# Optimization experiments

Measured on AMD Instinct MI355X. Metric: run time of the kernel, lower is better.

## Reference

```python
import jax, jax.numpy as jnp
import numpy as np

BS, NQ, NK = 2, 2048, 2048
D_OUT, H, D_K, D_V = 1024, 16, 64, 64


def _xavier(key, shape):
    fan_in, fan_out = shape[1], shape[0]
    lim = float(np.sqrt(6.0 / (fan_in + fan_out)))
    return jax.random.uniform(key, shape, jnp.float32, -lim, lim)


def setup_inputs() -> dict:
    key = jax.random.key(0)
    ks = jax.random.split(key, 9)
    return {
        "queries": jax.random.normal(ks[0], (BS, NQ, D_OUT), jnp.float32),
        "keys": jax.random.normal(ks[1], (BS, NK, D_OUT), jnp.float32),
        "values": jax.random.normal(ks[2], (BS, NK, D_OUT), jnp.float32),
        "mask": jax.random.randint(ks[3], (BS, H, NQ, NK), 0, 2).astype(bool),
        "weights": jax.random.uniform(ks[4], (BS, H, NQ, NK), jnp.float32),
        "Wq": _xavier(ks[5], (H * D_K, D_OUT)),
        "bq": jnp.zeros((H * D_K,), jnp.float32),
        "Wk": _xavier(ks[6], (H * D_K, D_OUT)),
        "bk": jnp.zeros((H * D_K,), jnp.float32),
        "Wv": _xavier(ks[7], (H * D_V, D_OUT)),
        "bv": jnp.zeros((H * D_V,), jnp.float32),
        "Wo": _xavier(ks[8], (D_OUT, H * D_V)),
        "bo": jnp.zeros((D_OUT,), jnp.float32),
    }


def reference(queries, keys, values, mask, weights, Wq, bq, Wk, bk, Wv, bv, Wo, bo):
    bs, nq, _ = queries.shape
    nk = keys.shape[1]
    # projections: (bs, n, h*d) -> (bs, h, n, d)
    q = (queries @ Wq.T + bq).reshape(bs, nq, H, D_K).transpose(0, 2, 1, 3)
    k = (keys @ Wk.T + bk).reshape(bs, nk, H, D_K).transpose(0, 2, 1, 3)
    v = (values @ Wv.T + bv).reshape(bs, nk, H, D_V).transpose(0, 2, 1, 3)
    # scaled dot-product scores: (bs, h, nq, nk)
    att = jnp.einsum("bhqd,bhkd->bhqk", q, k) / jnp.sqrt(jnp.float32(D_K))
    att = att * weights                      # elementwise weight bias
    att = jnp.where(mask, -jnp.inf, att)     # masked_fill(mask, -inf)
    att = jax.nn.softmax(att, axis=-1)
    # dropout is identity at p=0 / eval
    out = jnp.einsum("bhqk,bhkd->bhqd", att, v)  # (bs, h, nq, d_v)
    out = out.transpose(0, 2, 1, 3).reshape(bs, nq, H * D_V)
    return out @ Wo.T + bo
```

## Files before the change

### kernel.cpp

```cpp
#include <hip/hip_runtime.h>
#include <stdint.h>

#define DEV __device__ __forceinline__

typedef __attribute__((__ext_vector_type__(8))) short short8;
typedef __attribute__((__ext_vector_type__(4))) float f32x4;
typedef __attribute__((__ext_vector_type__(16))) float f32x16;
typedef __attribute__((__ext_vector_type__(4))) unsigned short ushort4_t;
typedef __attribute__((__ext_vector_type__(4))) _Float16 half4;
typedef __attribute__((__ext_vector_type__(8))) _Float16 half8;

DEV unsigned short f2bf(float f) {
  union { float f; unsigned u; } x; x.f = f;
  unsigned u = x.u;
  unsigned r = (u + 0x7FFFu + ((u >> 16) & 1u)) >> 16;
  return (unsigned short)r;
}

DEV unsigned short f2h(float f) {
  _Float16 h = (_Float16)f;
  unsigned short u;
  __builtin_memcpy(&u, &h, 2);
  return u;
}

DEV void gload_lds16(const void* g, void* l) {
  __builtin_amdgcn_global_load_lds(
      (const __attribute__((address_space(1))) unsigned int*)g,
      (__attribute__((address_space(3))) unsigned int*)l,
      16, 0, 0);
}

DEV short8 ld_g8(const unsigned short* p) { return *(const short8*)p; }
DEV short8 ld_s8(const unsigned short* p) { return *(const short8*)p; }
DEV half4 ld_h4(const unsigned short* p) {
  half4 r; __builtin_memcpy(&r, p, 8); return r;
}

__global__ void detect_mask_fmt(const unsigned int* __restrict__ mask, int* __restrict__ flag) {
  if (threadIdx.x == 0 && blockIdx.x == 0) {
    int fmt = 1;
    for (int i = 0; i < 256; ++i) {
      unsigned u = mask[i];
      if (u == 0x3F800000u) { fmt = 2; break; }
      if ((u & 0xFFFFFF00u) != 0u) { fmt = 0; break; }
    }
    *flag = fmt;
  }
}

__global__ void pack_mask(const unsigned char* __restrict__ m8,
                          const unsigned int* __restrict__ m32,
                          const int* __restrict__ mfmt,
                          unsigned int* __restrict__ pm) {
  __shared__ unsigned int tile[32 * 65];
  const int bh = blockIdx.x >> 6;
  const int q0 = (blockIdx.x & 63) * 32;
  const int fmt = *mfmt;
  const int tid = threadIdx.x;
#pragma unroll
  for (int rnd = 0; rnd < 8; ++rnd) {
    int w = tid + rnd * 256;
    int q = w >> 6, t = w & 63;
    size_t sb = ((size_t)(bh * 2048 + q0 + q)) * 2048 + t * 32;
    unsigned bits = 0;
    if (fmt == 0) {
      uint4 a = *(const uint4*)(m8 + sb);
      uint4 bq = *(const uint4*)(m8 + sb + 16);
      unsigned wa0 = a.x, wa1 = a.y, wa2 = a.z, wa3 = a.w;
      unsigned wb0 = bq.x, wb1 = bq.y, wb2 = bq.z, wb3 = bq.w;
#pragma unroll
      for (int e = 0; e < 4; ++e) {
        bits |= (((wa0 >> (8 * e)) & 0xFFu) ? 1u : 0u) << (0 + e);
        bits |= (((wa1 >> (8 * e)) & 0xFFu) ? 1u : 0u) << (4 + e);
        bits |= (((wa2 >> (8 * e)) & 0xFFu) ? 1u : 0u) << (8 + e);
        bits |= (((wa3 >> (8 * e)) & 0xFFu) ? 1u : 0u) << (12 + e);
        bits |= (((wb0 >> (8 * e)) & 0xFFu) ? 1u : 0u) << (16 + e);
        bits |= (((wb1 >> (8 * e)) & 0xFFu) ? 1u : 0u) << (20 + e);
        bits |= (((wb2 >> (8 * e)) & 0xFFu) ? 1u : 0u) << (24 + e);
        bits |= (((wb3 >> (8 * e)) & 0xFFu) ? 1u : 0u) << (28 + e);
      }
    } else {
#pragma unroll
      for (int c = 0; c < 8; ++c) {
        uint4 v = *(const uint4*)(m32 + sb + c * 4);
        bits |= (v.x ? 1u : 0u) << (c * 4);
        bits |= (v.y ? 1u : 0u) << (c * 4 + 1);
        bits |= (v.z ? 1u : 0u) << (c * 4 + 2);
        bits |= (v.w ? 1u : 0u) << (c * 4 + 3);
      }
    }
    tile[q * 65 + t] = bits;
  }
  __syncthreads();
#pragma unroll
  for (int rnd = 0; rnd < 8; ++rnd) {
    int w = tid + rnd * 256;
    int t = w >> 5, q = w & 31;
    pm[((size_t)bh * 64 + t) * 2048 + q0 + q] = tile[q * 65 + t];
  }
}

__global__ void cvt_all(const float* __restrict__ q, const float* __restrict__ k,
                        const float* __restrict__ v,
                        const float* __restrict__ wq, const float* __restrict__ wk,
                        const float* __restrict__ wv, const float* __restrict__ wo,
                        unsigned short* __restrict__ Xq, unsigned short* __restrict__ Xk,
                        unsigned short* __restrict__ Xv, unsigned short* __restrict__ Wqb,
                        unsigned short* __restrict__ Wkb, unsigned short* __restrict__ Wvb,
                        unsigned short* __restrict__ Wob) {
  int i = blockIdx.x * 256 + threadIdx.x;
  const float* src; unsigned short* dst; int off;
  if (i < 1048576)      { src = q;  dst = Xq;  off = i; }
  else if (i < 2097152) { src = k;  dst = Xk;  off = i - 1048576; }
  else if (i < 3145728) { src = v;  dst = Xv;  off = i - 2097152; }
  else if (i < 3407872) { src = wq; dst = Wqb; off = i - 3145728; }
  else if (i < 3670016) { src = wk; dst = Wkb; off = i - 3407872; }
  else if (i < 3932160) { src = wv; dst = Wvb; off = i - 3670016; }
  else                  { src = wo; dst = Wob; off = i - 3932160; }
  float4 vv = ((const float4*)src)[off];
  ushort4_t r;
  r.x = f2bf(vv.x); r.y = f2bf(vv.y); r.z = f2bf(vv.z); r.w = f2bf(vv.w);
  ((ushort4_t*)dst)[off] = r;
}

__global__ __launch_bounds__(256, 2) void proj_gemm(
    const unsigned short* __restrict__ Xq, const unsigned short* __restrict__ Xk,
    const unsigned short* __restrict__ Xv,
    const unsigned short* __restrict__ Wqb, const unsigned short* __restrict__ Wkb,
    const unsigned short* __restrict__ Wvb,
    const float* __restrict__ bq, const float* __restrict__ bk, const float* __restrict__ bv,
    unsigned short* __restrict__ QP, unsigned short* __restrict__ KP,
    unsigned short* __restrict__ VT) {
  const int tid = threadIdx.x;
// ... 30 lines not shown
    __syncthreads();

    short8 af[4], bfr[4];
#pragma unroll
    for (int i = 0; i < 4; ++i)
      af[i] = ld_s8(&stage[aoff + (wm + i * 16 + l16) * 32 + hi * 8]);
#pragma unroll
    for (int j = 0; j < 4; ++j)
      bfr[j] = ld_s8(&stage[boff + (wn + j * 16 + l16) * 32 + hi * 8]);
#pragma unroll
    for (int i = 0; i < 4; ++i)
#pragma unroll
      for (int j = 0; j < 4; ++j)
        acc[i][j] = __builtin_amdgcn_mfma_f32_16x16x32_bf16(af[i], bfr[j], acc[i][j], 0, 0, 0);
    __syncthreads();
  }

  if (sel != 2) {
#pragma unroll
    for (int j = 0; j < 4; ++j) {
      int feat = n0 + wn + j * 16 + l16;
      float bi = bias[feat];
      int h = feat >> 6, d = feat & 63;
#pragma unroll
      for (int i = 0; i < 4; ++i) {
#pragma unroll
        for (int r = 0; r < 4; ++r) {
          int m = m0 + wm + i * 16 + hi * 4 + r;
          int b = m >> 11, n = m & 2047;
          float v = acc[i][j][r] + bi;
          out[(((size_t)(b * 16 + h)) * 2048 + n) * 64 + d] = f2bf(v);
        }
      }
    }
  } else {
#pragma unroll
    for (int j = 0; j < 4; ++j) {
      int tc0 = m0 + wn + j * 16;
      int b = tc0 >> 11, n = tc0 & 2047;
#pragma unroll
      for (int i = 0; i < 4; ++i) {
#pragma unroll
        for (int r = 0; r < 4; ++r) {
          int feat = n0 + wm + i * 16 + hi * 4 + r;
          int h = feat >> 6, d = feat & 63;
          float v = acc[i][j][r] + bias[feat];
          out[((size_t)(b * 16 + h) * 64 + d) * 2048 + n + l16] = f2h(v);
        }
      }
    }
  }
}

__global__ __launch_bounds__(256, 2) void attn_kernel(
    const unsigned short* __restrict__ Q, const unsigned short* __restrict__ K,
    const unsigned short* __restrict__ VT,
    const float* __restrict__ weights,
    const unsigned int* __restrict__ pm,
    unsigned short* __restrict__ O) {
  const int bid = blockIdx.x;
  const int qt = bid >> 5, bh = bid & 31;
  const int b = bh >> 4, h = bh & 15;
  const int tid = threadIdx.x, wid = tid >> 6, lane = tid & 63;
  const int l31 = lane & 31, hh = lane >> 5;
  const size_t bh_nd = (size_t)bh * 2048 * 64;
  const int q0 = qt * 128;
  const int qg = q0 + wid * 32 + l31;

  short8 qf0 = ld_g8(Q + bh_nd + (size_t)qg * 64 + 0  + hh * 8);
  short8 qf1 = ld_g8(Q + bh_nd + (size_t)qg * 64 + 16 + hh * 8);
  short8 qf2 = ld_g8(Q + bh_nd + (size_t)qg * 64 + 32 + hh * 8);
  short8 qf3 = ld_g8(Q + bh_nd + (size_t)qg * 64 + 48 + hh * 8);

  __shared__ float wlds[2][128 * 32];
  __shared__ unsigned short vlds[2][64 * 32];

  const float* wsrc = weights + (size_t)bh * 2048 * 2048;
  const unsigned short* vsrc = VT + bh_nd;
  const int wswz = 4 * ((lane & 7) ^ (lane >> 3));
  const int vswz = 8 * ((lane & 3) ^ ((lane >> 3) & 3));
  const int wrow_s = q0 + wid * 32 + (lane >> 3);
  const int vrow_s = wid * 16 + (lane >> 2);

#define STAGE(NXT, KT)                                                        \
  {                                                                           \
    _Pragma("unroll")                                                         \
    for (int i = 0; i < 4; ++i)                                               \
      gload_lds16(wsrc + (size_t)(wrow_s + i * 8) * 2048 + (KT) + wswz,       \
                  &wlds[NXT][(wid * 4 + i) * 256]);                           \
    gload_lds16(vsrc + (size_t)vrow_s * 2048 + (KT) + vswz,                   \
                &vlds[NXT][wid * 512]);                                       \
  }

  f32x16 o0 = {}, o1 = {};
  float mrow = -1e30f, lrow = 0.f;

  STAGE(0, 0)
  __syncthreads();

  for (int t = 0; t < 64; ++t) {
    const int cur = t & 1;
    const int kt0 = t * 32;

    short8 kf0 = ld_g8(K + bh_nd + (size_t)(kt0 + l31) * 64 + 0  + hh * 8);
    short8 kf1 = ld_g8(K + bh_nd + (size_t)(kt0 + l31) * 64 + 16 + hh * 8);
    short8 kf2 = ld_g8(K + bh_nd + (size_t)(kt0 + l31) * 64 + 32 + hh * 8);
    short8 kf3 = ld_g8(K + bh_nd + (size_t)(kt0 + l31) * 64 + 48 + hh * 8);
    unsigned mw = pm[((size_t)bh * 64 + t) * 2048 + qg];

    if (t < 63) STAGE(cur ^ 1, kt0 + 32)

    f32x16 s = {};
    s = __builtin_amdgcn_mfma_f32_32x32x16_bf16(kf0, qf0, s, 0, 0, 0);
    s = __builtin_amdgcn_mfma_f32_32x32x16_bf16(kf1, qf1, s, 0, 0, 0);
    s = __builtin_amdgcn_mfma_f32_32x32x16_bf16(kf2, qf2, s, 0, 0, 0);
    s = __builtin_amdgcn_mfma_f32_32x32x16_bf16(kf3, qf3, s, 0, 0, 0);

    const float* wrow = &wlds[cur][(wid * 32 + l31) * 32];
    f32x4 wv[4];
    wv[0] = *(const f32x4*)&wrow[4 * ((hh + 0) ^ (l31 & 7))];
    wv[1] = *(const f32x4*)&wrow[4 * ((hh + 2) ^ (l31 & 7))];
    wv[2] = *(const f32x4*)&wrow[4 * ((hh + 4) ^ (l31 & 7))];
    wv[3] = *(const f32x4*)&wrow[4 * ((hh + 6) ^ (l31 & 7))];

    unsigned mb = mw >> (4 * hh);
#pragma unroll
    for (int r = 0; r < 16; ++r) {
      bool mk = (mb >> ((r & 3) + 8 * (r >> 2))) & 1;
      s[r] = mk ? -INFINITY : s[r] * 0.125f * wv[r >> 2][r & 3];
    }

    float tm = s[0];
#pragma unroll
    for (int r = 1; r < 16; ++r) tm = fmaxf(tm, s[r]);
    float tm2 = fmaxf(tm, __shfl_xor(tm, 32));
    if (__any(tm2 > mrow)) {
      float mnew = fmaxf(mrow, tm2);
      float sc = __expf(mrow - mnew);
      lrow *= sc;
      o0 *= sc;
      o1 *= sc;
      mrow = mnew;
    }
    float ps = 0.f;
#pragma unroll
    for (int r = 0; r < 16; ++r) {
      s[r] = __expf(s[r] - mrow);
      ps += s[r];
    }
    lrow += ps;

    half8 pa0, pa1;
#pragma unroll
    for (int r = 0; r < 8; ++r) {
      pa0[r] = (_Float16)s[r];
      pa1[r] = (_Float16)s[8 + r];
    }

    {
      const unsigned short* vr = &vlds[cur][l31 * 32];
      half4 a0 = ld_h4(&vr[4 * ((hh + 0) ^ (l31 & 6))]);
      half4 a1 = ld_h4(&vr[4 * ((hh + 2) ^ (l31 & 6))]);
      half8 vf;
#pragma unroll
      for (int e = 0; e < 4; ++e) { vf[e] = a0[e]; vf[4 + e] = a1[e]; }
      o0 = __builtin_amdgcn_mfma_f32_32x32x16_f16(vf, pa0, o0, 0, 0, 0);
      half4 b0 = ld_h4(&vr[4 * ((hh + 4) ^ (l31 & 6))]);
      half4 b1 = ld_h4(&vr[4 * ((hh + 6) ^ (l31 & 6))]);
#pragma unroll
      for (int e = 0; e < 4; ++e) { vf[e] = b0[e]; vf[4 + e] = b1[e]; }
      o0 = __builtin_amdgcn_mfma_f32_32x32x16_f16(vf, pa1, o0, 0, 0, 0);
    }
    {
      const unsigned short* vr = &vlds[cur][(32 + l31) * 32];
      half4 a0 = ld_h4(&vr[4 * ((hh + 0) ^ (l31 & 6))]);
      half4 a1 = ld_h4(&vr[4 * ((hh + 2) ^ (l31 & 6))]);
      half8 vf;
#pragma unroll
      for (int e = 0; e < 4; ++e) { vf[e] = a0[e]; vf[4 + e] = a1[e]; }
      o1 = __builtin_amdgcn_mfma_f32_32x32x16_f16(vf, pa0, o1, 0, 0, 0);
      half4 b0 = ld_h4(&vr[4 * ((hh + 4) ^ (l31 & 6))]);
      half4 b1 = ld_h4(&vr[4 * ((hh + 6) ^ (l31 & 6))]);
#pragma unroll
      for (int e = 0; e < 4; ++e) { vf[e] = b0[e]; vf[4 + e] = b1[e]; }
      o1 = __builtin_amdgcn_mfma_f32_32x32x16_f16(vf, pa1, o1, 0, 0, 0);
    }

    __syncthreads();
  }

  lrow += __shfl_xor(lrow, 32);
  float inv = 1.0f / lrow;
  const size_t ob = (size_t)(b * 2048 + qg) * 1024 + h * 64;
#pragma unroll
  for (int j = 0; j < 4; ++j) {
    ushort4_t pk;
    pk.x = f2bf(o0[4 * j + 0] * inv); pk.y = f2bf(o0[4 * j + 1] * inv);
    pk.z = f2bf(o0[4 * j + 2] * inv); pk.w = f2bf(o0[4 * j + 3] * inv);
    *(ushort4_t*)&O[ob + 8 * j + 4 * hh] = pk;
    ushort4_t pk1;
    pk1.x = f2bf(o1[4 * j + 0] * inv); pk1.y = f2bf(o1[4 * j + 1] * inv);
    pk1.z = f2bf(o1[4 * j + 2] * inv); pk1.w = f2bf(o1[4 * j + 3] * inv);
    *(ushort4_t*)&O[ob + 32 + 8 * j + 4 * hh] = pk1;
  }
#undef STAGE
}

__global__ __launch_bounds__(256, 2) void out_gemm(
    const unsigned short* __restrict__ A, const unsigned short* __restrict__ W,
    const float* __restrict__ bias, float* __restrict__ Cout) {
  const int tid = threadIdx.x;
  const int wid = tid >> 6, lane = tid & 63;
  const int l16 = lane & 15, hi = lane >> 4;
  const int m0 = blockIdx.x * 128;
  const int n0 = blockIdx.y * 128;

  __shared__ unsigned short stage[2 * 128 * 32];
  f32x4 acc[4][4] = {};
  const int wm = (wid >> 1) * 64, wn = (wid & 1) * 64;

  for (int kt = 0; kt < 1024; kt += 32) {
#pragma unroll
    for (int t = 0; t < 4; ++t) {
      int g = wid * 4 + t;
      int c = g & 7;
      int row = c * 16 + (lane >> 2);
      int ko = (lane & 3) * 8;
      const unsigned short* src = (g < 8)
          ? (A + (size_t)(m0 + row) * 1024 + kt + ko)
          : (W + (size_t)(n0 + row) * 1024 + kt + ko);
      gload_lds16(src, (unsigned short*)((char*)stage + g * 1024));
    }
    __syncthreads();

    short8 af[4], bfr[4];
#pragma unroll
    for (int i = 0; i < 4; ++i)
      af[i] = ld_s8(&stage[(wm + i * 16 + l16) * 32 + hi * 8]);
#pragma unroll
    for (int j = 0; j < 4; ++j)
      bfr[j] = ld_s8(&stage[4096 + (wn + j * 16 + l16) * 32 + hi * 8]);
#pragma unroll
    for (int i = 0; i < 4; ++i)
#pragma unroll
      for (int j = 0; j < 4; ++j)
        acc[i][j] = __builtin_amdgcn_mfma_f32_16x16x32_bf16(af[i], bfr[j], acc[i][j], 0, 0, 0);
    __syncthreads();
  }

#pragma unroll
  for (int j = 0; j < 4; ++j) {
    int feat = n0 + wn + j * 16 + l16;
    float bi = bias[feat];
#pragma unroll
    for (int i = 0; i < 4; ++i) {
#pragma unroll
      for (int r = 0; r < 4; ++r) {
        int m = m0 + wm + i * 16 + hi * 4 + r;
        Cout[(size_t)m * 1024 + feat] = acc[i][j][r] + bi;
      }
    }
  }
}

extern "C" void kernel_launch(void* const* d_in, const int* in_sizes, int n_in,
                              void* d_out, int out_size, void* d_ws, size_t ws_size,
                              hipStream_t stream) {
  const float* queries = (const float*)d_in[0];
  const float* keys    = (const float*)d_in[1];
  const float* values  = (const float*)d_in[2];
  const void*  maskp   = d_in[3];
  const float* weights = (const float*)d_in[4];
  const float* Wq = (const float*)d_in[5];
  const float* bq = (const float*)d_in[6];
  const float* Wk = (const float*)d_in[7];
  const float* bk = (const float*)d_in[8];
  const float* Wv = (const float*)d_in[9];
  const float* bv = (const float*)d_in[10];
  const float* Wo = (const float*)d_in[11];
  const float* bo = (const float*)d_in[12];

  unsigned short* ws = (unsigned short*)d_ws;
  unsigned short* Xq  = ws;
  unsigned short* Xk  = ws + 4194304;
  unsigned short* Xv  = ws + 8388608;
  unsigned short* Wqb = ws + 12582912;
  unsigned short* Wkb = ws + 13631488;
  unsigned short* Wvb = ws + 14680064;
  unsigned short* Wob = ws + 15728640;
  unsigned short* QP  = ws + 16777216;
  unsigned short* KP  = ws + 20971520;
  unsigned short* VPT = ws + 25165824;
  unsigned short* OB  = Xq;
  unsigned int* pmb   = (unsigned int*)(ws + 4194304);
  int* mflag = (int*)(ws + 29360128);

  detect_mask_fmt<<<1, 64, 0, stream>>>((const unsigned int*)maskp, mflag);

  cvt_all<<<16384, 256, 0, stream>>>(queries, keys, values, Wq, Wk, Wv, Wo,
                                     Xq, Xk, Xv, Wqb, Wkb, Wvb, Wob);

  proj_gemm<<<dim3(32, 24), 256, 0, stream>>>(Xq, Xk, Xv, Wqb, Wkb, Wvb,
                                              bq, bk, bv, QP, KP, VPT);

  pack_mask<<<2048, 256, 0, stream>>>((const unsigned char*)maskp,
                                      (const unsigned int*)maskp, mflag, pmb);

  attn_kernel<<<512, 256, 0, stream>>>(QP, KP, VPT, weights, pmb, OB);

  out_gemm<<<dim3(32, 8), 256, 0, stream>>>(OB, Wob, bo, (float*)d_out);
}
```

Before: 359.2 us.

## Deepen attention prefetch to a 4-buffer LDS ring with register double-buffered K

Widens the weights/V LDS staging from double to quad buffering and prefetches two tiles ahead. K fragments and mask words are now loaded one iteration early into alternating register sets. A manual vmcnt wait and a single s_barrier per iteration replace the trailing __syncthreads, so memory latency can overlap more compute. The cost is roughly double the LDS footprint, more live registers, and a few redundant wrapped loads on the final iterations.

```diff
diff --git a/kernel.cpp b/kernel.cpp
--- a/kernel.cpp
+++ b/kernel.cpp
@@ -236,121 +236,138 @@
   short8 qf2 = ld_g8(Q + bh_nd + (size_t)qg * 64 + 32 + hh * 8);
   short8 qf3 = ld_g8(Q + bh_nd + (size_t)qg * 64 + 48 + hh * 8);
 
-  __shared__ float wlds[2][128 * 32];
-  __shared__ unsigned short vlds[2][64 * 32];
+  __shared__ float wlds[4][128 * 32];
+  __shared__ unsigned short vlds[4][64 * 32];
 
   const float* wsrc = weights + (size_t)bh * 2048 * 2048;
   const unsigned short* vsrc = VT + bh_nd;
+  const unsigned short* ksrc = K + bh_nd;
+  const unsigned int* pmsrc = pm + (size_t)bh * 64 * 2048 + qg;
   const int wswz = 4 * ((lane & 7) ^ (lane >> 3));
   const int vswz = 8 * ((lane & 3) ^ ((lane >> 3) & 3));
   const int wrow_s = q0 + wid * 32 + (lane >> 3);
   const int vrow_s = wid * 16 + (lane >> 2);
 
-#define STAGE(NXT, KT)                                                        \
+#define STAGE(BUF, KT)                                                        \
   {                                                                           \
     _Pragma("unroll")                                                         \
-    for (int i = 0; i < 4; ++i)                                               \
-      gload_lds16(wsrc + (size_t)(wrow_s + i * 8) * 2048 + (KT) + wswz,       \
-                  &wlds[NXT][(wid * 4 + i) * 256]);                           \
+    for (int i_ = 0; i_ < 4; ++i_)                                            \
+      gload_lds16(wsrc + (size_t)(wrow_s + i_ * 8) * 2048 + (KT) + wswz,      \
+                  &wlds[BUF][(wid * 4 + i_) * 256]);                          \
     gload_lds16(vsrc + (size_t)vrow_s * 2048 + (KT) + vswz,                   \
-                &vlds[NXT][wid * 512]);                                       \
+                &vlds[BUF][wid * 512]);                                       \
+  }
+
+#define LOADK(K0, K1, K2, K3, PM, T)                                          \
+  {                                                                           \
+    const int kt_ = (T) * 32;                                                 \
+    K0 = ld_g8(ksrc + (size_t)(kt_ + l31) * 64 + 0  + hh * 8);                \
+    K1 = ld_g8(ksrc + (size_t)(kt_ + l31) * 64 + 16 + hh * 8);                \
+    K2 = ld_g8(ksrc + (size_t)(kt_ + l31) * 64 + 32 + hh * 8);                \
+    K3 = ld_g8(ksrc + (size_t)(kt_ + l31) * 64 + 48 + hh * 8);                \
+    PM = pmsrc[(size_t)(T) * 2048];                                           \
   }
 
   f32x16 o0 = {}, o1 = {};
   float mrow = -1e30f, lrow = 0.f;
+  short8 ka0, ka1, ka2, ka3, kb0, kb1, kb2, kb3;
+  unsigned pma, pmb;
 
   STAGE(0, 0)
-  __syncthreads();
-
-  for (int t = 0; t < 64; ++t) {
-    const int cur = t & 1;
-    const int kt0 = t * 32;
-
-    short8 kf0 = ld_g8(K + bh_nd + (size_t)(kt0 + l31) * 64 + 0  + hh * 8);
-    short8 kf1 = ld_g8(K + bh_nd + (size_t)(kt0 + l31) * 64 + 16 + hh * 8);
-    short8 kf2 = ld_g8(K + bh_nd + (size_t)(kt0 + l31) * 64 + 32 + hh * 8);
-    short8 kf3 = ld_g8(K + bh_nd + (size_t)(kt0 + l31) * 64 + 48 + hh * 8);
-    unsigned mw = pm[((size_t)bh * 64 + t) * 2048 + qg];
-
-    if (t < 63) STAGE(cur ^ 1, kt0 + 32)
-
-    f32x16 s = {};
-    s = __builtin_amdgcn_mfma_f32_32x32x16_bf16(kf0, qf0, s, 0, 0, 0);
-    s = __builtin_amdgcn_mfma_f32_32x32x16_bf16(kf1, qf1, s, 0, 0, 0);
-    s = __builtin_amdgcn_mfma_f32_32x32x16_bf16(kf2, qf2, s, 0, 0, 0);
-    s = __builtin_amdgcn_mfma_f32_32x32x16_bf16(kf3, qf3, s, 0, 0, 0);
-
-    const float* wrow = &wlds[cur][(wid * 32 + l31) * 32];
-    f32x4 wv[4];
-    wv[0] = *(const f32x4*)&wrow[4 * ((hh + 0) ^ (l31 & 7))];
-    wv[1] = *(const f32x4*)&wrow[4 * ((hh + 2) ^ (l31 & 7))];
-    wv[2] = *(const f32x4*)&wrow[4 * ((hh + 4) ^ (l31 & 7))];
-    wv[3] = *(const f32x4*)&wrow[4 * ((hh + 6) ^ (l31 & 7))];
-
-    unsigned mb = mw >> (4 * hh);
-#pragma unroll
-    for (int r = 0; r < 16; ++r) {
-      bool mk = (mb >> ((r & 3) + 8 * (r >> 2))) & 1;
-      s[r] = mk ? -INFINITY : s[r] * 0.125f * wv[r >> 2][r & 3];
-    }
-
-    float tm = s[0];
-#pragma unroll
-    for (int r = 1; r < 16; ++r) tm = fmaxf(tm, s[r]);
-    float tm2 = fmaxf(tm, __shfl_xor(tm, 32));
-    if (__any(tm2 > mrow)) {
-      float mnew = fmaxf(mrow, tm2);
-      float sc = __expf(mrow - mnew);
-      lrow *= sc;
-      o0 *= sc;
-      o1 *= sc;
-      mrow = mnew;
-    }
-    float ps = 0.f;
-#pragma unroll
-    for (int r = 0; r < 16; ++r) {
-      s[r] = __expf(s[r] - mrow);
-      ps += s[r];
-    }
-    lrow += ps;
-
-    half8 pa0, pa1;
-#pragma unroll
-    for (int r = 0; r < 8; ++r) {
-      pa0[r] = (_Float16)s[r];
-      pa1[r] = (_Float16)s[8 + r];
-    }
-
-    {
-      const unsigned short* vr = &vlds[cur][l31 * 32];
-      half4 a0 = ld_h4(&vr[4 * ((hh + 0) ^ (l31 & 6))]);
-      half4 a1 = ld_h4(&vr[4 * ((hh + 2) ^ (l31 & 6))]);
-      half8 vf;
-#pragma unroll
-      for (int e = 0; e < 4; ++e) { vf[e] = a0[e]; vf[4 + e] = a1[e]; }
-      o0 = __builtin_amdgcn_mfma_f32_32x32x16_f16(vf, pa0, o0, 0, 0, 0);
-      half4 b0 = ld_h4(&vr[4 * ((hh + 4) ^ (l31 & 6))]);
-      half4 b1 = ld_h4(&vr[4 * ((hh + 6) ^ (l31 & 6))]);
-#pragma unroll
-      for (int e = 0; e < 4; ++e) { vf[e] = b0[e]; vf[4 + e] = b1[e]; }
-      o0 = __builtin_amdgcn_mfma_f32_32x32x16_f16(vf, pa1, o0, 0, 0, 0);
-    }
-    {
-      const unsigned short* vr = &vlds[cur][(32 + l31) * 32];
-      half4 a0 = ld_h4(&vr[4 * ((hh + 0) ^ (l31 & 6))]);
-      half4 a1 = ld_h4(&vr[4 * ((hh + 2) ^ (l31 & 6))]);
-      half8 vf;
-#pragma unroll
-      for (int e = 0; e < 4; ++e) { vf[e] = a0[e]; vf[4 + e] = a1[e]; }
-      o1 = __builtin_amdgcn_mfma_f32_32x32x16_f16(vf, pa0, o1, 0, 0, 0);
-      half4 b0 = ld_h4(&vr[4 * ((hh + 4) ^ (l31 & 6))]);
-      half4 b1 = ld_h4(&vr[4 * ((hh + 6) ^ (l31 & 6))]);
-#pragma unroll
-      for (int e = 0; e < 4; ++e) { vf[e] = b0[e]; vf[4 + e] = b1[e]; }
-      o1 = __builtin_amdgcn_mfma_f32_32x32x16_f16(vf, pa1, o1, 0, 0, 0);
-    }
-
-    __syncthreads();
+  LOADK(ka0, ka1, ka2, ka3, pma, 0)
+  STAGE(1, 32)
+
+#define ITER(T, KC0, KC1, KC2, KC3, PMC, KN0, KN1, KN2, KN3, PMN)             \
+  {                                                                           \
+    const int t1_ = ((T) + 1) & 63, t2_ = ((T) + 2) & 63;                     \
+    LOADK(KN0, KN1, KN2, KN3, PMN, t1_)                                       \
+    __builtin_amdgcn_sched_barrier(0);                                        \
+    STAGE(((T) + 2) & 3, t2_ * 32)                                            \
+    __builtin_amdgcn_sched_barrier(0);                                        \
+    asm volatile("s_waitcnt vmcnt(15)" ::: "memory");                         \
+    __builtin_amdgcn_s_barrier();                                             \
+    __builtin_amdgcn_sched_barrier(0);                                        \
+    const int cur_ = (T) & 3;                                                 \
+                                                              \
+    f32x16 s = {};                                                            \
+    s = __builtin_amdgcn_mfma_f32_32x32x16_bf16(KC0, qf0, s, 0, 0, 0);        \
+    s = __builtin_amdgcn_mfma_f32_32x32x16_bf16(KC1, qf1, s, 0, 0, 0);        \
+    s = __builtin_amdgcn_mfma_f32_32x32x16_bf16(KC2, qf2, s, 0, 0, 0);        \
+    s = __builtin_amdgcn_mfma_f32_32x32x16_bf16(KC3, qf3, s, 0, 0, 0);        \
+                                                          \
+    const float* wrow_ = &wlds[cur_][(wid * 32 + l31) * 32];                  \
+    f32x4 wv_[4];                                                             \
+    wv_[0] = *(const f32x4*)&wrow_[4 * ((hh + 0) ^ (l31 & 7))];               \
+    wv_[1] = *(const f32x4*)&wrow_[4 * ((hh + 2) ^ (l31 & 7))];               \
+    wv_[2] = *(const f32x4*)&wrow_[4 * ((hh + 4) ^ (l31 & 7))];               \
+    wv_[3] = *(const f32x4*)&wrow_[4 * ((hh + 6) ^ (l31 & 7))];               \
+    unsigned mb_ = (PMC) >> (4 * hh);                                         \
+    _Pragma("unroll")                                                         \
+    for (int r = 0; r < 16; ++r) {                                            \
+      bool mk = (mb_ >> ((r & 3) + 8 * (r >> 2))) & 1;                        \
+      s[r] = mk ? -INFINITY : s[r] * 0.125f * wv_[r >> 2][r & 3];             \
+    }                                                                         \
+                                                          \
+    float tm = s[0];                                                          \
+    _Pragma("unroll")                                                         \
+    for (int r = 1; r < 16; ++r) tm = fmaxf(tm, s[r]);                        \
+    float tm2 = fmaxf(tm, __shfl_xor(tm, 32));                                \
+    if (__any(tm2 > mrow)) {                                                  \
+      float mnew = fmaxf(mrow, tm2);                                          \
+      float sc = __expf(mrow - mnew);                                         \
+      lrow *= sc;                                                             \
+      o0 *= sc;                                                               \
+      o1 *= sc;                                                               \
+      mrow = mnew;                                                            \
+    }                                                                         \
+    float ps = 0.f;                                                           \
+    _Pragma("unroll")                                                         \
+    for (int r = 0; r < 16; ++r) {                                            \
+      s[r] = __expf(s[r] - mrow);                                             \
+      ps += s[r];                                                             \
+    }                                                                         \
+    lrow += ps;                                                               \
+                                                             \
+    half8 pa0, pa1;                                                           \
+    _Pragma("unroll")                                                         \
+    for (int r = 0; r < 8; ++r) {                                             \
+      pa0[r] = (_Float16)s[r];                                                \
+      pa1[r] = (_Float16)s[8 + r];                                            \
+    }                                                                         \
+                                                                      \
+    {                                                                         \
+      const unsigned short* vr_ = &vlds[cur_][l31 * 32];                      \
+      half4 a0 = ld_h4(&vr_[4 * ((hh + 0) ^ (l31 & 6))]);                     \
+      half4 a1 = ld_h4(&vr_[4 * ((hh + 2) ^ (l31 & 6))]);                     \
+      half8 vf;                                                               \
+      _Pragma("unroll")                                                       \
+      for (int e = 0; e < 4; ++e) { vf[e] = a0[e]; vf[4 + e] = a1[e]; }       \
+      o0 = __builtin_amdgcn_mfma_f32_32x32x16_f16(vf, pa0, o0, 0, 0, 0);      \
+      half4 b0 = ld_h4(&vr_[4 * ((hh + 4) ^ (l31 & 6))]);                     \
+      half4 b1 = ld_h4(&vr_[4 * ((hh + 6) ^ (l31 & 6))]);                     \
+      _Pragma("unroll")                                                       \
+      for (int e = 0; e < 4; ++e) { vf[e] = b0[e]; vf[4 + e] = b1[e]; }       \
+      o0 = __builtin_amdgcn_mfma_f32_32x32x16_f16(vf, pa1, o0, 0, 0, 0);      \
+    }                                                                         \
+    {                                                                         \
+      const unsigned short* vr_ = &vlds[cur_][(32 + l31) * 32];               \
+      half4 a0 = ld_h4(&vr_[4 * ((hh + 0) ^ (l31 & 6))]);                     \
+      half4 a1 = ld_h4(&vr_[4 * ((hh + 2) ^ (l31 & 6))]);                     \
+      half8 vf;                                                               \
+      _Pragma("unroll")                                                       \
+      for (int e = 0; e < 4; ++e) { vf[e] = a0[e]; vf[4 + e] = a1[e]; }       \
+      o1 = __builtin_amdgcn_mfma_f32_32x32x16_f16(vf, pa0, o1, 0, 0, 0);      \
+      half4 b0 = ld_h4(&vr_[4 * ((hh + 4) ^ (l31 & 6))]);                     \
+      half4 b1 = ld_h4(&vr_[4 * ((hh + 6) ^ (l31 & 6))]);                     \
+      _Pragma("unroll")                                                       \
+      for (int e = 0; e < 4; ++e) { vf[e] = b0[e]; vf[4 + e] = b1[e]; }       \
+      o1 = __builtin_amdgcn_mfma_f32_32x32x16_f16(vf, pa1, o1, 0, 0, 0);      \
+    }                                                                         \
+  }
+
+  for (int t = 0; t < 64; t += 2) {
+    ITER(t,     ka0, ka1, ka2, ka3, pma, kb0, kb1, kb2, kb3, pmb)
+    ITER(t + 1, kb0, kb1, kb2, kb3, pmb, ka0, ka1, ka2, ka3, pma)
   }
 
   lrow += __shfl_xor(lrow, 32);
@@ -367,6 +384,8 @@
     pk1.z = f2bf(o1[4 * j + 2] * inv); pk1.w = f2bf(o1[4 * j + 3] * inv);
     *(ushort4_t*)&O[ob + 32 + 8 * j + 4 * hh] = pk1;
   }
+#undef ITER
+#undef LOADK
 #undef STAGE
 }
 
```

After: 362.0 us. No clear change (+0.8%).

## Split attention key range across waves with LDS merge of softmax partials

Applied to the files above, without the earlier changes.

The attention kernel now uses 512 threads per block over 64 query rows. Eight waves split as two query halves times four key quarters, each walking 256-key chunks with the weights tile staged into 128 KB of LDS. K and V fragments are loaded straight from global memory into registers instead of staging V through LDS, with explicit waitcnt and barriers for double buffering. The partial outputs and running max/sum are merged through LDS at the end. This aims to raise parallelism and cut per-iteration barrier overhead, at the cost of large LDS use limiting occupancy, a final reduction step, and redundant K/V global reads across query halves.

```diff
diff --git a/kernel.cpp b/kernel.cpp
--- a/kernel.cpp
+++ b/kernel.cpp
@@ -216,7 +216,7 @@
   }
 }
 
-__global__ __launch_bounds__(256, 2) void attn_kernel(
+__global__ __launch_bounds__(512, 2) void attn_kernel(
     const unsigned short* __restrict__ Q, const unsigned short* __restrict__ K,
     const unsigned short* __restrict__ VT,
     const float* __restrict__ weights,
@@ -225,147 +225,191 @@
   const int bid = blockIdx.x;
   const int qt = bid >> 5, bh = bid & 31;
   const int b = bh >> 4, h = bh & 15;
-  const int tid = threadIdx.x, wid = tid >> 6, lane = tid & 63;
+  const int tid = threadIdx.x;
+  const int wv8 = tid >> 6, lane = tid & 63;
   const int l31 = lane & 31, hh = lane >> 5;
+  const int qh = wv8 >> 2, kq = wv8 & 3;
   const size_t bh_nd = (size_t)bh * 2048 * 64;
-  const int q0 = qt * 128;
-  const int qg = q0 + wid * 32 + l31;
+  const int qg = qt * 64 + qh * 32 + l31;
 
   short8 qf0 = ld_g8(Q + bh_nd + (size_t)qg * 64 + 0  + hh * 8);
   short8 qf1 = ld_g8(Q + bh_nd + (size_t)qg * 64 + 16 + hh * 8);
   short8 qf2 = ld_g8(Q + bh_nd + (size_t)qg * 64 + 32 + hh * 8);
   short8 qf3 = ld_g8(Q + bh_nd + (size_t)qg * 64 + 48 + hh * 8);
 
-  __shared__ float wlds[2][128 * 32];
-  __shared__ unsigned short vlds[2][64 * 32];
+  __shared__ float wlds[2][64 * 256];
 
   const float* wsrc = weights + (size_t)bh * 2048 * 2048;
   const unsigned short* vsrc = VT + bh_nd;
-  const int wswz = 4 * ((lane & 7) ^ (lane >> 3));
-  const int vswz = 8 * ((lane & 3) ^ ((lane >> 3) & 3));
-  const int wrow_s = q0 + wid * 32 + (lane >> 3);
-  const int vrow_s = wid * 16 + (lane >> 2);
-
-#define STAGE(NXT, KT)                                                        \
+  const unsigned short* ksrc = K + bh_nd;
+  const unsigned int* pmsrc = pm + (size_t)(bh * 64) * 2048 + qg;
+
+#define STAGE(BB, TT)                                                         \
   {                                                                           \
     _Pragma("unroll")                                                         \
-    for (int i = 0; i < 4; ++i)                                               \
-      gload_lds16(wsrc + (size_t)(wrow_s + i * 8) * 2048 + (KT) + wswz,       \
-                  &wlds[NXT][(wid * 4 + i) * 256]);                           \
-    gload_lds16(vsrc + (size_t)vrow_s * 2048 + (KT) + vswz,                   \
-                &vlds[NXT][wid * 512]);                                       \
+    for (int i_ = 0; i_ < 8; ++i_) {                                          \
+      const int c_ = wv8 * 8 + i_;                                            \
+      gload_lds16(wsrc + (size_t)(qt * 64 + c_) * 2048 + (TT) * 256           \
+                      + 4 * (lane ^ (c_ & 31)),                               \
+                  &wlds[BB][c_ * 256]);                                       \
+    }                                                                         \
   }
 
   f32x16 o0 = {}, o1 = {};
   float mrow = -1e30f, lrow = 0.f;
 
   STAGE(0, 0)
+
+  for (int t = 0; t < 8; ++t) {
+    const int cb = t & 1;
+
+    short8 kf[2][4];
+    half4 vva[2][4], vvb[2][4];
+    unsigned pmw[2];
+#pragma unroll
+    for (int s = 0; s < 2; ++s) {
+      const int k0 = t * 256 + kq * 64 + s * 32;
+#pragma unroll
+      for (int j = 0; j < 4; ++j)
+        kf[s][j] = ld_g8(ksrc + (size_t)(k0 + l31) * 64 + 16 * j + 8 * hh);
+#pragma unroll
+      for (int cc = 0; cc < 4; ++cc) {
+        vva[s][cc] = ld_h4(vsrc + (size_t)l31 * 2048 + k0 + 4 * hh + 8 * cc);
+        vvb[s][cc] = ld_h4(vsrc + (size_t)(32 + l31) * 2048 + k0 + 4 * hh + 8 * cc);
+      }
+      pmw[s] = pmsrc[(size_t)(t * 8 + kq * 2 + s) * 2048];
+    }
+    __builtin_amdgcn_sched_barrier(0);
+
+    if (t < 7) {
+      STAGE(cb ^ 1, t + 1)
+      __builtin_amdgcn_sched_barrier(0);
+      asm volatile("s_waitcnt vmcnt(8)" ::: "memory");
+    } else {
+      asm volatile("s_waitcnt vmcnt(0)" ::: "memory");
+    }
+    __builtin_amdgcn_s_barrier();
+    __builtin_amdgcn_sched_barrier(0);
+
+#pragma unroll
+    for (int s = 0; s < 2; ++s) {
+      f32x16 sv = {};
+      sv = __builtin_amdgcn_mfma_f32_32x32x16_bf16(kf[s][0], qf0, sv, 0, 0, 0);
+      sv = __builtin_amdgcn_mfma_f32_32x32x16_bf16(kf[s][1], qf1, sv, 0, 0, 0);
+      sv = __builtin_amdgcn_mfma_f32_32x32x16_bf16(kf[s][2], qf2, sv, 0, 0, 0);
+      sv = __builtin_amdgcn_mfma_f32_32x32x16_bf16(kf[s][3], qf3, sv, 0, 0, 0);
+
+      const float* wb = &wlds[cb][(qh * 32 + l31) * 256];
+      f32x4 wv4[4];
+#pragma unroll
+      for (int cc = 0; cc < 4; ++cc) {
+        int u = (kq * 16 + s * 8 + 2 * cc + hh) ^ l31;
+        wv4[cc] = *(const f32x4*)&wb[4 * u];
+      }
+      unsigned mb = pmw[s] >> (4 * hh);
+#pragma unroll
+      for (int r = 0; r < 16; ++r) {
+        bool mk = (mb >> ((r & 3) + 8 * (r >> 2))) & 1;
+        sv[r] = mk ? -INFINITY : sv[r] * 0.125f * wv4[r >> 2][r & 3];
+      }
+
+      float tm = sv[0];
+#pragma unroll
+      for (int r = 1; r < 16; ++r) tm = fmaxf(tm, sv[r]);
+      float tm2 = fmaxf(tm, __shfl_xor(tm, 32));
+      if (__any(tm2 > mrow)) {
+        float mnew = fmaxf(mrow, tm2);
+        float sc = __expf(mrow - mnew);
+        lrow *= sc;
+        o0 *= sc;
+        o1 *= sc;
+        mrow = mnew;
+      }
+      float ps = 0.f;
+#pragma unroll
+      for (int r = 0; r < 16; ++r) {
+        sv[r] = __expf(sv[r] - mrow);
+        ps += sv[r];
+      }
+      lrow += ps;
+
+      half8 pa0, pa1;
+#pragma unroll
+      for (int r = 0; r < 8; ++r) {
+        pa0[r] = (_Float16)sv[r];
+        pa1[r] = (_Float16)sv[8 + r];
+      }
+
+      {
+        half8 vf;
+#pragma unroll
+        for (int e = 0; e < 4; ++e) { vf[e] = vva[s][0][e]; vf[4 + e] = vva[s][1][e]; }
+        o0 = __builtin_amdgcn_mfma_f32_32x32x16_f16(vf, pa0, o0, 0, 0, 0);
+#pragma unroll
+        for (int e = 0; e < 4; ++e) { vf[e] = vva[s][2][e]; vf[4 + e] = vva[s][3][e]; }
+        o0 = __builtin_amdgcn_mfma_f32_32x32x16_f16(vf, pa1, o0, 0, 0, 0);
+#pragma unroll
+        for (int e = 0; e < 4; ++e) { vf[e] = vvb[s][0][e]; vf[4 + e] = vvb[s][1][e]; }
+        o1 = __builtin_amdgcn_mfma_f32_32x32x16_f16(vf, pa0, o1, 0, 0, 0);
+#pragma unroll
+        for (int e = 0; e < 4; ++e) { vf[e] = vvb[s][2][e]; vf[4 + e] = vvb[s][3][e]; }
+        o1 = __builtin_amdgcn_mfma_f32_32x32x16_f16(vf, pa1, o1, 0, 0, 0);
+      }
+    }
+
+    asm volatile("s_waitcnt lgkmcnt(0)" ::: "memory");
+    __builtin_amdgcn_s_barrier();
+    __builtin_amdgcn_sched_barrier(0);
+  }
+
+  lrow += __shfl_xor(lrow, 32);
+  float* pb = &wlds[0][0];
+  float* mlb = pb + 256 * 68;
+  const int prow = (qh * 4 + kq) * 32 + l31;
+#pragma unroll
+  for (int j = 0; j < 4; ++j) {
+    f32x4 a0 = { o0[4 * j], o0[4 * j + 1], o0[4 * j + 2], o0[4 * j + 3] };
+    f32x4 a1 = { o1[4 * j], o1[4 * j + 1], o1[4 * j + 2], o1[4 * j + 3] };
+    *(f32x4*)&pb[prow * 68 + 8 * j + 4 * hh] = a0;
+    *(f32x4*)&pb[prow * 68 + 32 + 8 * j + 4 * hh] = a1;
+  }
+  if (hh == 0) {
+    mlb[prow] = mrow;
+    mlb[256 + prow] = lrow;
+  }
   __syncthreads();
 
-  for (int t = 0; t < 64; ++t) {
-    const int cur = t & 1;
-    const int kt0 = t * 32;
-
-    short8 kf0 = ld_g8(K + bh_nd + (size_t)(kt0 + l31) * 64 + 0  + hh * 8);
-    short8 kf1 = ld_g8(K + bh_nd + (size_t)(kt0 + l31) * 64 + 16 + hh * 8);
-    short8 kf2 = ld_g8(K + bh_nd + (size_t)(kt0 + l31) * 64 + 32 + hh * 8);
-    short8 kf3 = ld_g8(K + bh_nd + (size_t)(kt0 + l31) * 64 + 48 + hh * 8);
-    unsigned mw = pm[((size_t)bh * 64 + t) * 2048 + qg];
-
-    if (t < 63) STAGE(cur ^ 1, kt0 + 32)
-
-    f32x16 s = {};
-    s = __builtin_amdgcn_mfma_f32_32x32x16_bf16(kf0, qf0, s, 0, 0, 0);
-    s = __builtin_amdgcn_mfma_f32_32x32x16_bf16(kf1, qf1, s, 0, 0, 0);
-    s = __builtin_amdgcn_mfma_f32_32x32x16_bf16(kf2, qf2, s, 0, 0, 0);
-    s = __builtin_amdgcn_mfma_f32_32x32x16_bf16(kf3, qf3, s, 0, 0, 0);
-
-    const float* wrow = &wlds[cur][(wid * 32 + l31) * 32];
-    f32x4 wv[4];
-    wv[0] = *(const f32x4*)&wrow[4 * ((hh + 0) ^ (l31 & 7))];
-    wv[1] = *(const f32x4*)&wrow[4 * ((hh + 2) ^ (l31 & 7))];
-    wv[2] = *(const f32x4*)&wrow[4 * ((hh + 4) ^ (l31 & 7))];
-    wv[3] = *(const f32x4*)&wrow[4 * ((hh + 6) ^ (l31 & 7))];
-
-    unsigned mb = mw >> (4 * hh);
-#pragma unroll
-    for (int r = 0; r < 16; ++r) {
-      bool mk = (mb >> ((r & 3) + 8 * (r >> 2))) & 1;
-      s[r] = mk ? -INFINITY : s[r] * 0.125f * wv[r >> 2][r & 3];
-    }
-
-    float tm = s[0];
-#pragma unroll
-    for (int r = 1; r < 16; ++r) tm = fmaxf(tm, s[r]);
-    float tm2 = fmaxf(tm, __shfl_xor(tm, 32));
-    if (__any(tm2 > mrow)) {
-      float mnew = fmaxf(mrow, tm2);
-      float sc = __expf(mrow - mnew);
-      lrow *= sc;
-      o0 *= sc;
-      o1 *= sc;
-      mrow = mnew;
-    }
-    float ps = 0.f;
-#pragma unroll
-    for (int r = 0; r < 16; ++r) {
-      s[r] = __expf(s[r] - mrow);
-      ps += s[r];
-    }
-    lrow += ps;
-
-    half8 pa0, pa1;
-#pragma unroll
-    for (int r = 0; r < 8; ++r) {
-      pa0[r] = (_Float16)s[r];
-      pa1[r] = (_Float16)s[8 + r];
-    }
-
-    {
-      const unsigned short* vr = &vlds[cur][l31 * 32];
-      half4 a0 = ld_h4(&vr[4 * ((hh + 0) ^ (l31 & 6))]);
-      half4 a1 = ld_h4(&vr[4 * ((hh + 2) ^ (l31 & 6))]);
-      half8 vf;
-#pragma unroll
-      for (int e = 0; e < 4; ++e) { vf[e] = a0[e]; vf[4 + e] = a1[e]; }
-      o0 = __builtin_amdgcn_mfma_f32_32x32x16_f16(vf, pa0, o0, 0, 0, 0);
-      half4 b0 = ld_h4(&vr[4 * ((hh + 4) ^ (l31 & 6))]);
-      half4 b1 = ld_h4(&vr[4 * ((hh + 6) ^ (l31 & 6))]);
-#pragma unroll
-      for (int e = 0; e < 4; ++e) { vf[e] = b0[e]; vf[4 + e] = b1[e]; }
-      o0 = __builtin_amdgcn_mfma_f32_32x32x16_f16(vf, pa1, o0, 0, 0, 0);
-    }
-    {
-      const unsigned short* vr = &vlds[cur][(32 + l31) * 32];
-      half4 a0 = ld_h4(&vr[4 * ((hh + 0) ^ (l31 & 6))]);
-      half4 a1 = ld_h4(&vr[4 * ((hh + 2) ^ (l31 & 6))]);
-      half8 vf;
-#pragma unroll
-      for (int e = 0; e < 4; ++e) { vf[e] = a0[e]; vf[4 + e] = a1[e]; }
-      o1 = __builtin_amdgcn_mfma_f32_32x32x16_f16(vf, pa0, o1, 0, 0, 0);
-      half4 b0 = ld_h4(&vr[4 * ((hh + 4) ^ (l31 & 6))]);
-      half4 b1 = ld_h4(&vr[4 * ((hh + 6) ^ (l31 & 6))]);
-#pragma unroll
-      for (int e = 0; e < 4; ++e) { vf[e] = b0[e]; vf[4 + e] = b1[e]; }
-      o1 = __builtin_amdgcn_mfma_f32_32x32x16_f16(vf, pa1, o1, 0, 0, 0);
-    }
-
-    __syncthreads();
-  }
-
-  lrow += __shfl_xor(lrow, 32);
-  float inv = 1.0f / lrow;
-  const size_t ob = (size_t)(b * 2048 + qg) * 1024 + h * 64;
-#pragma unroll
-  for (int j = 0; j < 4; ++j) {
-    ushort4_t pk;
-    pk.x = f2bf(o0[4 * j + 0] * inv); pk.y = f2bf(o0[4 * j + 1] * inv);
-    pk.z = f2bf(o0[4 * j + 2] * inv); pk.w = f2bf(o0[4 * j + 3] * inv);
-    *(ushort4_t*)&O[ob + 8 * j + 4 * hh] = pk;
-    ushort4_t pk1;
-    pk1.x = f2bf(o1[4 * j + 0] * inv); pk1.y = f2bf(o1[4 * j + 1] * inv);
-    pk1.z = f2bf(o1[4 * j + 2] * inv); pk1.w = f2bf(o1[4 * j + 3] * inv);
-    *(ushort4_t*)&O[ob + 32 + 8 * j + 4 * hh] = pk1;
+  if (kq == 0) {
+    float mg[4], lg[4];
+#pragma unroll
+    for (int g = 0; g < 4; ++g) {
+      mg[g] = mlb[(qh * 4 + g) * 32 + l31];
+      lg[g] = mlb[256 + (qh * 4 + g) * 32 + l31];
+    }
+    float M = fmaxf(fmaxf(mg[0], mg[1]), fmaxf(mg[2], mg[3]));
+    float cg[4], L = 0.f;
+#pragma unroll
+    for (int g = 0; g < 4; ++g) { cg[g] = __expf(mg[g] - M); L += cg[g] * lg[g]; }
+    float inv = 1.0f / L;
+    const size_t ob = (size_t)(b * 2048 + qg) * 1024 + h * 64;
+#pragma unroll
+    for (int j = 0; j < 4; ++j) {
+      f32x4 a0 = {}, a1 = {};
+#pragma unroll
+      for (int g = 0; g < 4; ++g) {
+        int pr = (qh * 4 + g) * 32 + l31;
+        a0 += cg[g] * (*(const f32x4*)&pb[pr * 68 + 8 * j + 4 * hh]);
+        a1 += cg[g] * (*(const f32x4*)&pb[pr * 68 + 32 + 8 * j + 4 * hh]);
+      }
+      ushort4_t pk;
+      pk.x = f2bf(a0[0] * inv); pk.y = f2bf(a0[1] * inv);
+      pk.z = f2bf(a0[2] * inv); pk.w = f2bf(a0[3] * inv);
+      *(ushort4_t*)&O[ob + 8 * j + 4 * hh] = pk;
+      ushort4_t pk1;
+      pk1.x = f2bf(a1[0] * inv); pk1.y = f2bf(a1[1] * inv);
+      pk1.z = f2bf(a1[2] * inv); pk1.w = f2bf(a1[3] * inv);
+      *(ushort4_t*)&O[ob + 32 + 8 * j + 4 * hh] = pk1;
+    }
   }
 #undef STAGE
 }
@@ -470,7 +514,7 @@
   pack_mask<<<2048, 256, 0, stream>>>((const unsigned char*)maskp,
                                       (const unsigned int*)maskp, mflag, pmb);
 
-  attn_kernel<<<512, 256, 0, stream>>>(QP, KP, VPT, weights, pmb, OB);
+  attn_kernel<<<1024, 512, 0, stream>>>(QP, KP, VPT, weights, pmb, OB);
 
   out_gemm<<<dim3(32, 8), 256, 0, stream>>>(OB, Wob, bo, (float*)d_out);
 }
```

After: 487.3 us. 35.7% more time.

## Split attention key range across wave pairs and merge partial softmax results

Applied to the files above, without the earlier changes.

The attention kernel now uses 64-query tiles with 1024 blocks. Within each block, two wave pairs each process half of the key range, and their partial max/sum/output are merged through LDS at the end (split-K flash attention). V is loaded straight from global memory into registers instead of being staged through LDS, and the per-iteration block barrier is replaced by an explicit vmcnt wait. Launch bounds are raised to four blocks per CU to increase occupancy. The packed-mask buffer moves to a separate workspace region. The risks are higher register pressure, uncoalesced V loads, and a hand-tuned vmcnt count that could be fragile.

```diff
diff --git a/kernel.cpp b/kernel.cpp
--- a/kernel.cpp
+++ b/kernel.cpp
@@ -67,19 +67,12 @@
     if (fmt == 0) {
       uint4 a = *(const uint4*)(m8 + sb);
       uint4 bq = *(const uint4*)(m8 + sb + 16);
-      unsigned wa0 = a.x, wa1 = a.y, wa2 = a.z, wa3 = a.w;
-      unsigned wb0 = bq.x, wb1 = bq.y, wb2 = bq.z, wb3 = bq.w;
-#pragma unroll
-      for (int e = 0; e < 4; ++e) {
-        bits |= (((wa0 >> (8 * e)) & 0xFFu) ? 1u : 0u) << (0 + e);
-        bits |= (((wa1 >> (8 * e)) & 0xFFu) ? 1u : 0u) << (4 + e);
-        bits |= (((wa2 >> (8 * e)) & 0xFFu) ? 1u : 0u) << (8 + e);
-        bits |= (((wa3 >> (8 * e)) & 0xFFu) ? 1u : 0u) << (12 + e);
-        bits |= (((wb0 >> (8 * e)) & 0xFFu) ? 1u : 0u) << (16 + e);
-        bits |= (((wb1 >> (8 * e)) & 0xFFu) ? 1u : 0u) << (20 + e);
-        bits |= (((wb2 >> (8 * e)) & 0xFFu) ? 1u : 0u) << (24 + e);
-        bits |= (((wb3 >> (8 * e)) & 0xFFu) ? 1u : 0u) << (28 + e);
-      }
+      unsigned wa[8] = {a.x, a.y, a.z, a.w, bq.x, bq.y, bq.z, bq.w};
+#pragma unroll
+      for (int c = 0; c < 8; ++c)
+#pragma unroll
+        for (int e = 0; e < 4; ++e)
+          bits |= (((wa[c] >> (8 * e)) & 0xFFu) ? 1u : 0u) << (c * 4 + e);
     } else {
 #pragma unroll
       for (int c = 0; c < 8; ++c) {
@@ -216,7 +209,7 @@
   }
 }
 
-__global__ __launch_bounds__(256, 2) void attn_kernel(
+__global__ __launch_bounds__(256, 4) void attn_kernel(
     const unsigned short* __restrict__ Q, const unsigned short* __restrict__ K,
     const unsigned short* __restrict__ VT,
     const float* __restrict__ weights,
@@ -225,54 +218,63 @@
   const int bid = blockIdx.x;
   const int qt = bid >> 5, bh = bid & 31;
   const int b = bh >> 4, h = bh & 15;
-  const int tid = threadIdx.x, wid = tid >> 6, lane = tid & 63;
+  const int tid = threadIdx.x;
+  const int w4 = tid >> 6, lane = tid & 63;
+  const int qh = w4 & 1, ks = w4 >> 1;
   const int l31 = lane & 31, hh = lane >> 5;
   const size_t bh_nd = (size_t)bh * 2048 * 64;
-  const int q0 = qt * 128;
-  const int qg = q0 + wid * 32 + l31;
+  const int q0 = qt * 64;
+  const int qg = q0 + qh * 32 + l31;
 
   short8 qf0 = ld_g8(Q + bh_nd + (size_t)qg * 64 + 0  + hh * 8);
   short8 qf1 = ld_g8(Q + bh_nd + (size_t)qg * 64 + 16 + hh * 8);
   short8 qf2 = ld_g8(Q + bh_nd + (size_t)qg * 64 + 32 + hh * 8);
   short8 qf3 = ld_g8(Q + bh_nd + (size_t)qg * 64 + 48 + hh * 8);
 
-  __shared__ float wlds[2][128 * 32];
-  __shared__ unsigned short vlds[2][64 * 32];
+  __shared__ float wlds[2][2][64 * 32];
+  __shared__ float mlbuf[128];
 
   const float* wsrc = weights + (size_t)bh * 2048 * 2048;
   const unsigned short* vsrc = VT + bh_nd;
+  const unsigned short* ksrc = K + bh_nd;
+  const unsigned int* pmsrc = pm + (size_t)(bh * 64) * 2048 + qg;
   const int wswz = 4 * ((lane & 7) ^ (lane >> 3));
-  const int vswz = 8 * ((lane & 3) ^ ((lane >> 3) & 3));
-  const int wrow_s = q0 + wid * 32 + (lane >> 3);
-  const int vrow_s = wid * 16 + (lane >> 2);
-
-#define STAGE(NXT, KT)                                                        \
+  const int wrow_s = q0 + qh * 32 + (lane >> 3);
+
+#define STAGE(NXT, KTILE)                                                     \
   {                                                                           \
     _Pragma("unroll")                                                         \
-    for (int i = 0; i < 4; ++i)                                               \
-      gload_lds16(wsrc + (size_t)(wrow_s + i * 8) * 2048 + (KT) + wswz,       \
-                  &wlds[NXT][(wid * 4 + i) * 256]);                           \
-    gload_lds16(vsrc + (size_t)vrow_s * 2048 + (KT) + vswz,                   \
-                &vlds[NXT][wid * 512]);                                       \
+    for (int i_ = 0; i_ < 4; ++i_)                                            \
+      gload_lds16(wsrc + (size_t)(wrow_s + i_ * 8) * 2048                     \
+                      + (size_t)(KTILE) * 32 + wswz,                          \
+                  &wlds[ks][NXT][(qh * 32 + i_ * 8) * 32]);                   \
   }
 
   f32x16 o0 = {}, o1 = {};
   float mrow = -1e30f, lrow = 0.f;
 
-  STAGE(0, 0)
-  __syncthreads();
-
-  for (int t = 0; t < 64; ++t) {
+  STAGE(0, ks * 32)
+
+  for (int t = 0; t < 32; ++t) {
     const int cur = t & 1;
-    const int kt0 = t * 32;
-
-    short8 kf0 = ld_g8(K + bh_nd + (size_t)(kt0 + l31) * 64 + 0  + hh * 8);
-    short8 kf1 = ld_g8(K + bh_nd + (size_t)(kt0 + l31) * 64 + 16 + hh * 8);
-    short8 kf2 = ld_g8(K + bh_nd + (size_t)(kt0 + l31) * 64 + 32 + hh * 8);
-    short8 kf3 = ld_g8(K + bh_nd + (size_t)(kt0 + l31) * 64 + 48 + hh * 8);
-    unsigned mw = pm[((size_t)bh * 64 + t) * 2048 + qg];
-
-    if (t < 63) STAGE(cur ^ 1, kt0 + 32)
+    const int ktile = ks * 32 + t;
+    const int kt0 = ktile * 32;
+
+    short8 kf0 = ld_g8(ksrc + (size_t)(kt0 + l31) * 64 + 0  + hh * 8);
+    short8 kf1 = ld_g8(ksrc + (size_t)(kt0 + l31) * 64 + 16 + hh * 8);
+    short8 kf2 = ld_g8(ksrc + (size_t)(kt0 + l31) * 64 + 32 + hh * 8);
+    short8 kf3 = ld_g8(ksrc + (size_t)(kt0 + l31) * 64 + 48 + hh * 8);
+    unsigned mw = pmsrc[(size_t)ktile * 2048];
+    half4 vva[4], vvb[4];
+#pragma unroll
+    for (int cc = 0; cc < 4; ++cc) {
+      vva[cc] = ld_h4(vsrc + (size_t)l31 * 2048 + kt0 + 4 * hh + 8 * cc);
+      vvb[cc] = ld_h4(vsrc + (size_t)(32 + l31) * 2048 + kt0 + 4 * hh + 8 * cc);
+    }
+
+    if (t < 31) STAGE(cur ^ 1, ktile + 1)
+
+    asm volatile("s_waitcnt vmcnt(13)" ::: "memory");
 
     f32x16 s = {};
     s = __builtin_amdgcn_mfma_f32_32x32x16_bf16(kf0, qf0, s, 0, 0, 0);
@@ -280,7 +282,7 @@
     s = __builtin_amdgcn_mfma_f32_32x32x16_bf16(kf2, qf2, s, 0, 0, 0);
     s = __builtin_amdgcn_mfma_f32_32x32x16_bf16(kf3, qf3, s, 0, 0, 0);
 
-    const float* wrow = &wlds[cur][(wid * 32 + l31) * 32];
+    const float* wrow = &wlds[ks][cur][(qh * 32 + l31) * 32];
     f32x4 wv[4];
     wv[0] = *(const f32x4*)&wrow[4 * ((hh + 0) ^ (l31 & 7))];
     wv[1] = *(const f32x4*)&wrow[4 * ((hh + 2) ^ (l31 & 7))];
@@ -322,50 +324,60 @@
     }
 
     {
-      const unsigned short* vr = &vlds[cur][l31 * 32];
-      half4 a0 = ld_h4(&vr[4 * ((hh + 0) ^ (l31 & 6))]);
-      half4 a1 = ld_h4(&vr[4 * ((hh + 2) ^ (l31 & 6))]);
       half8 vf;
 #pragma unroll
-      for (int e = 0; e < 4; ++e) { vf[e] = a0[e]; vf[4 + e] = a1[e]; }
+      for (int e = 0; e < 4; ++e) { vf[e] = vva[0][e]; vf[4 + e] = vva[1][e]; }
       o0 = __builtin_amdgcn_mfma_f32_32x32x16_f16(vf, pa0, o0, 0, 0, 0);
-      half4 b0 = ld_h4(&vr[4 * ((hh + 4) ^ (l31 & 6))]);
-      half4 b1 = ld_h4(&vr[4 * ((hh + 6) ^ (l31 & 6))]);
-#pragma unroll
-      for (int e = 0; e < 4; ++e) { vf[e] = b0[e]; vf[4 + e] = b1[e]; }
+#pragma unroll
+      for (int e = 0; e < 4; ++e) { vf[e] = vva[2][e]; vf[4 + e] = vva[3][e]; }
       o0 = __builtin_amdgcn_mfma_f32_32x32x16_f16(vf, pa1, o0, 0, 0, 0);
-    }
-    {
-      const unsigned short* vr = &vlds[cur][(32 + l31) * 32];
-      half4 a0 = ld_h4(&vr[4 * ((hh + 0) ^ (l31 & 6))]);
-      half4 a1 = ld_h4(&vr[4 * ((hh + 2) ^ (l31 & 6))]);
-      half8 vf;
-#pragma unroll
-      for (int e = 0; e < 4; ++e) { vf[e] = a0[e]; vf[4 + e] = a1[e]; }
+#pragma unroll
+      for (int e = 0; e < 4; ++e) { vf[e] = vvb[0][e]; vf[4 + e] = vvb[1][e]; }
       o1 = __builtin_amdgcn_mfma_f32_32x32x16_f16(vf, pa0, o1, 0, 0, 0);
-      half4 b0 = ld_h4(&vr[4 * ((hh + 4) ^ (l31 & 6))]);
-      half4 b1 = ld_h4(&vr[4 * ((hh + 6) ^ (l31 & 6))]);
-#pragma unroll
-      for (int e = 0; e < 4; ++e) { vf[e] = b0[e]; vf[4 + e] = b1[e]; }
+#pragma unroll
+      for (int e = 0; e < 4; ++e) { vf[e] = vvb[2][e]; vf[4 + e] = vvb[3][e]; }
       o1 = __builtin_amdgcn_mfma_f32_32x32x16_f16(vf, pa1, o1, 0, 0, 0);
     }
-
-    __syncthreads();
   }
 
   lrow += __shfl_xor(lrow, 32);
-  float inv = 1.0f / lrow;
-  const size_t ob = (size_t)(b * 2048 + qg) * 1024 + h * 64;
-#pragma unroll
-  for (int j = 0; j < 4; ++j) {
-    ushort4_t pk;
-    pk.x = f2bf(o0[4 * j + 0] * inv); pk.y = f2bf(o0[4 * j + 1] * inv);
-    pk.z = f2bf(o0[4 * j + 2] * inv); pk.w = f2bf(o0[4 * j + 3] * inv);
-    *(ushort4_t*)&O[ob + 8 * j + 4 * hh] = pk;
-    ushort4_t pk1;
-    pk1.x = f2bf(o1[4 * j + 0] * inv); pk1.y = f2bf(o1[4 * j + 1] * inv);
-    pk1.z = f2bf(o1[4 * j + 2] * inv); pk1.w = f2bf(o1[4 * j + 3] * inv);
-    *(ushort4_t*)&O[ob + 32 + 8 * j + 4 * hh] = pk1;
+  const int prow = qh * 32 + l31;
+  __syncthreads();
+  float* pb = &wlds[0][0][0];
+  if (ks == 1) {
+#pragma unroll
+    for (int j = 0; j < 4; ++j) {
+      f32x4 a0 = { o0[4 * j], o0[4 * j + 1], o0[4 * j + 2], o0[4 * j + 3] };
+      f32x4 a1 = { o1[4 * j], o1[4 * j + 1], o1[4 * j + 2], o1[4 * j + 3] };
+      *(f32x4*)&pb[prow * 64 + 8 * j + 4 * hh] = a0;
+      *(f32x4*)&pb[prow * 64 + 32 + 8 * j + 4 * hh] = a1;
+    }
+    if (hh == 0) { mlbuf[prow] = mrow; mlbuf[64 + prow] = lrow; }
+  }
+  __syncthreads();
+  if (ks == 0) {
+    float m1 = mlbuf[prow], l1 = mlbuf[64 + prow];
+    float M = fmaxf(mrow, m1);
+    float c0 = __expf(mrow - M), c1 = __expf(m1 - M);
+    float inv = 1.0f / (c0 * lrow + c1 * l1);
+    const size_t ob = (size_t)(b * 2048 + qg) * 1024 + h * 64;
+#pragma unroll
+    for (int j = 0; j < 4; ++j) {
+      f32x4 p0 = *(const f32x4*)&pb[prow * 64 + 8 * j + 4 * hh];
+      f32x4 p1 = *(const f32x4*)&pb[prow * 64 + 32 + 8 * j + 4 * hh];
+      ushort4_t pk;
+      pk.x = f2bf((c0 * o0[4 * j + 0] + c1 * p0[0]) * inv);
+      pk.y = f2bf((c0 * o0[4 * j + 1] + c1 * p0[1]) * inv);
+      pk.z = f2bf((c0 * o0[4 * j + 2] + c1 * p0[2]) * inv);
+      pk.w = f2bf((c0 * o0[4 * j + 3] + c1 * p0[3]) * inv);
+      *(ushort4_t*)&O[ob + 8 * j + 4 * hh] = pk;
+      ushort4_t pk1;
+      pk1.x = f2bf((c0 * o1[4 * j + 0] + c1 * p1[0]) * inv);
+      pk1.y = f2bf((c0 * o1[4 * j + 1] + c1 * p1[1]) * inv);
+      pk1.z = f2bf((c0 * o1[4 * j + 2] + c1 * p1[2]) * inv);
+      pk1.w = f2bf((c0 * o1[4 * j + 3] + c1 * p1[3]) * inv);
+      *(ushort4_t*)&O[ob + 32 + 8 * j + 4 * hh] = pk1;
+    }
   }
 #undef STAGE
 }
@@ -456,8 +468,8 @@
   unsigned short* KP  = ws + 20971520;
   unsigned short* VPT = ws + 25165824;
   unsigned short* OB  = Xq;
-  unsigned int* pmb   = (unsigned int*)(ws + 4194304);
   int* mflag = (int*)(ws + 29360128);
+  unsigned int* pmb   = (unsigned int*)(ws + 33554432);
 
   detect_mask_fmt<<<1, 64, 0, stream>>>((const unsigned int*)maskp, mflag);
 
@@ -470,7 +482,7 @@
   pack_mask<<<2048, 256, 0, stream>>>((const unsigned char*)maskp,
                                       (const unsigned int*)maskp, mflag, pmb);
 
-  attn_kernel<<<512, 256, 0, stream>>>(QP, KP, VPT, weights, pmb, OB);
+  attn_kernel<<<1024, 256, 0, stream>>>(QP, KP, VPT, weights, pmb, OB);
 
   out_gemm<<<dim3(32, 8), 256, 0, stream>>>(OB, Wob, bo, (float*)d_out);
 }
```

After: 458.3 us. +27.6%, slower.
